# Optimization experiments

Hardware: AMD Instinct MI355X
Metric: run time of the kernel (lower is better)

Reference implementation:

```python
import jax, jax.numpy as jnp
import numpy as np

B, L, D = 32, 2048, 1024
EPS = 1e-5


def setup_inputs() -> dict:
    key = jax.random.key(0)
    k = jax.random.split(key, 4)
    target_mask = jax.random.randint(k[0], (B, L), 0, 2, dtype=jnp.int64)
    x = jax.random.normal(k[1], (B, L, D), dtype=jnp.float32)
    # targets are zeroed out in context (per docstring); makes num_context logic real
    x = x * (1 - target_mask)[:, :, None].astype(jnp.float32)
    W1 = jax.random.normal(k[2], (D, 2 * D), dtype=jnp.float32) * 0.02
    W2 = jax.random.normal(k[3], (2 * D, D), dtype=jnp.float32) * 0.02
    return {
        "context_repr": x,
        "target_mask": target_mask,
        "W1": W1,
        "b1": jnp.zeros((2 * D,), jnp.float32),
        "gamma": jnp.ones((2 * D,), jnp.float32),
        "beta": jnp.zeros((2 * D,), jnp.float32),
        "W2": W2,
        "b2": jnp.zeros((D,), jnp.float32),
    }


def _mlp(x, W1, b1, gamma, beta, W2, b2):
    h = x @ W1 + b1                       # [B, 2D]
    h = jax.nn.gelu(h, approximate=False)  # torch default GELU (erf)
    mu = jnp.mean(h, axis=-1, keepdims=True)
    var = jnp.mean(jnp.square(h - mu), axis=-1, keepdims=True)
    h = (h - mu) * jax.lax.rsqrt(var + EPS) * gamma + beta
    return h @ W2 + b2                    # [B, D]


def reference(context_repr, target_mask, W1, b1, gamma, beta, W2, b2):
    b, l, d = context_repr.shape
    # num_targets is data-dependent but concrete here (eager), matching torch .item()
    ntgt = jnp.sum(target_mask, axis=1)              # [B]
    num_targets = int(jnp.max(ntgt))
    if num_targets == 0:
        return jnp.zeros((b, 1, d), dtype=context_repr.dtype)
    # per-batch masked mean pool: count rows with nonzero L1 norm
    num_ctx = jnp.sum(jnp.sum(jnp.abs(context_repr), axis=-1) > 0, axis=1)  # [B]
    denom = jnp.maximum(num_ctx, 1).astype(context_repr.dtype)[:, None]
    mean = jnp.sum(context_repr, axis=1) / denom
    mean = jnp.where((num_ctx > 0)[:, None], mean, jnp.zeros_like(mean))
    pred = _mlp(mean, W1, b1, gamma, beta, W2, b2)   # [B, D]
    valid = jnp.arange(num_targets)[None, :] < ntgt[:, None]  # [B, T]
    return jnp.where(valid[:, :, None], pred[:, None, :], 0.0)
```

## Files before the change

### kernel.cpp

```cpp
#include <hip/hip_runtime.h>
#include <math.h>

#define BATCH 32
#define LSEQ  2048
#define DIM   1024
#define DIM2  2048

constexpr float EPSF = 1e-5f;

constexpr int CHUNKS = 64;

constexpr int KSEG1 = 32;
constexpr int NSEG1 = DIM / KSEG1;
constexpr int KSEG2 = 32;
constexpr int NSEG2 = DIM2 / KSEG2;

typedef float f4v __attribute__((ext_vector_type(4)));

__global__ __launch_bounds__(256) void k0_compact(const int* __restrict__ m32,
                                                  int* __restrict__ rowlist,
                                                  int* __restrict__ cnt,
                                                  int* __restrict__ ntgt) {
    const int b    = blockIdx.x;
    const int t    = threadIdx.x;
    const int wave = t >> 6, lane = t & 63;

    const int probe = m32[(size_t)b * 2048 + 8 * t + 1];
    __shared__ unsigned long long pbw[4];
    const unsigned long long pb = __ballot(probe != 0);
    if (lane == 0) pbw[wave] = pb;
    __syncthreads();
    const int stride = ((pbw[0] | pbw[1] | pbw[2] | pbw[3]) != 0ull) ? 1 : 2;

    const int base = t * 8;
    int f[8];
    int ls = 0;
    #pragma unroll
    for (int k = 0; k < 8; ++k) {
        f[k] = (m32[((size_t)b * 2048 + base + k) * (size_t)stride] == 0) ? 1 : 0;
        ls += f[k];
    }

    int v = ls;
    #pragma unroll
    for (int o = 1; o < 64; o <<= 1) {
        const int u = __shfl_up(v, o, 64);
        if (lane >= o) v += u;
    }
    __shared__ int wsum[4];
    if (lane == 63) wsum[wave] = v;
    __syncthreads();
    int wbase = 0;
    for (int w = 0; w < wave; ++w) wbase += wsum[w];
    const int excl = wbase + v - ls;

    int c = 0;
    #pragma unroll
    for (int k = 0; k < 8; ++k) {
        if (f[k]) { rowlist[(size_t)b * 2048 + excl + c] = base + k; ++c; }
    }
    if (t == 0) {
        const int tot = wsum[0] + wsum[1] + wsum[2] + wsum[3];
        cnt[b]  = tot;
        ntgt[b] = LSEQ - tot;
    }
}

__global__ __launch_bounds__(256) void k1_gather(const float* __restrict__ x,
                                                 const int* __restrict__ rowlist,
                                                 const int* __restrict__ cnt,
                                                 float* __restrict__ psum) {
    const int chunk = blockIdx.x;
    const int b     = blockIdx.y;
    const int t     = threadIdx.x;

    const int cntb = cnt[b];
    const int nch  = (cntb + 31) >> 5;
    if (chunk >= nch) return;
    const int rbeg = chunk * 32;
    const int rcnt = min(32, cntb - rbeg);

    __shared__ int sidx[32];
    if (t < rcnt) sidx[t] = rowlist[(size_t)b * 2048 + rbeg + t];
    __syncthreads();

    const float* xb = x + (size_t)b * LSEQ * DIM + t * 4;
    float4 acc = make_float4(0.f, 0.f, 0.f, 0.f);

    if (rcnt == 32) {
        #pragma unroll 8
        for (int r = 0; r < 32; ++r) {
            const float4 v = *(const float4*)(xb + (size_t)sidx[r] * DIM);
            acc.x += v.x; acc.y += v.y; acc.z += v.z; acc.w += v.w;
        }
    } else {
        for (int r = 0; r < rcnt; ++r) {
            const float4 v = *(const float4*)(xb + (size_t)sidx[r] * DIM);
            acc.x += v.x; acc.y += v.y; acc.z += v.z; acc.w += v.w;
        }
    }

    *(float4*)(psum + ((size_t)b * CHUNKS + chunk) * DIM + t * 4) = acc;
}

__global__ __launch_bounds__(256) void k2_mean(const float* __restrict__ psum,
                                               const int* __restrict__ cnt,
                                               float* __restrict__ mean) {
    const int b = blockIdx.x;
    const int t = threadIdx.x;
    const int cntb = cnt[b];
    const int nch  = (cntb + 31) >> 5;

    float4 s = make_float4(0.f, 0.f, 0.f, 0.f);
    for (int c = 0; c < nch; ++c) {
        const float4 v = *(const float4*)(psum + ((size_t)b * CHUNKS + c) * DIM + t * 4);
        s.x += v.x; s.y += v.y; s.z += v.z; s.w += v.w;
    }
    const float denom = (float)(cntb > 1 ? cntb : 1);
    float4 m4;
    m4.x = s.x / denom; m4.y = s.y / denom; m4.z = s.z / denom; m4.w = s.w / denom;
    *(float4*)(mean + (size_t)b * DIM + t * 4) = m4;
}

__global__ __launch_bounds__(256) void k3a_h(const float* __restrict__ mean,
                                             const float* __restrict__ W1,
                                             float* __restrict__ p1) {
    const int j  = blockIdx.x * 256 + threadIdx.x;
    const int ks = blockIdx.y;
    const int k0 = ks * KSEG1;

    __shared__ float mlds[BATCH][KSEG1];
    for (int i = threadIdx.x; i < BATCH * KSEG1; i += 256)
        mlds[i >> 5][i & 31] = mean[(size_t)(i >> 5) * DIM + k0 + (i & 31)];
    __syncthreads();

    float acc[BATCH];
    #pragma unroll
    for (int b = 0; b < BATCH; ++b) acc[b] = 0.f;

    #pragma unroll
    for (int k4 = 0; k4 < KSEG1 / 4; ++k4) {
        const float w0 = W1[(size_t)(k0 + 4 * k4 + 0) * DIM2 + j];
        const float w1 = W1[(size_t)(k0 + 4 * k4 + 1) * DIM2 + j];
        const float w2 = W1[(size_t)(k0 + 4 * k4 + 2) * DIM2 + j];
        const float w3 = W1[(size_t)(k0 + 4 * k4 + 3) * DIM2 + j];
        #pragma unroll
        for (int b = 0; b < BATCH; ++b) {
            const float4 m4 = *(const float4*)&mlds[b][k4 * 4];
            acc[b] += m4.x * w0; acc[b] += m4.y * w1;
            acc[b] += m4.z * w2; acc[b] += m4.w * w3;
        }
    }
    #pragma unroll
    for (int b = 0; b < BATCH; ++b)
        p1[((size_t)ks * BATCH + b) * DIM2 + j] = acc[b];
}

__device__ __forceinline__ float wave_sum(float v) {
    #pragma unroll
    for (int o = 32; o > 0; o >>= 1) v += __shfl_down(v, o, 64);
    return v;
}

__global__ __launch_bounds__(256) void k3b_ln(const float* __restrict__ p1,
                                              const float* __restrict__ b1,
                                              const float* __restrict__ gamma,
                                              const float* __restrict__ beta,
                                              float* __restrict__ hn) {
    const int b = blockIdx.x;
    const int t = threadIdx.x;
    const int wave = t >> 6, lane = t & 63;
    __shared__ float red[4];

    float g[8];
    float ls = 0.f;
    #pragma unroll
    for (int i = 0; i < 8; ++i) {
        const int j = t + i * 256;
        float s = b1[j];
        #pragma unroll 8
        for (int ks = 0; ks < NSEG1; ++ks)
            s += p1[((size_t)ks * BATCH + b) * DIM2 + j];
        const float ge = 0.5f * s * (1.f + erff(s * 0.70710678118654752f));
        g[i] = ge;
        ls += ge;
    }

    float w = wave_sum(ls);
    if (lane == 0) red[wave] = w;
    __syncthreads();
    const float mu = (red[0] + red[1] + red[2] + red[3]) * (1.f / (float)DIM2);
    __syncthreads();

    float lv = 0.f;
    #pragma unroll
    for (int i = 0; i < 8; ++i) { const float d = g[i] - mu; lv += d * d; }
    w = wave_sum(lv);
    if (lane == 0) red[wave] = w;
    __syncthreads();
    const float var = (red[0] + red[1] + red[2] + red[3]) * (1.f / (float)DIM2);
    const float rs = rsqrtf(var + EPSF);

    #pragma unroll
    for (int i = 0; i < 8; ++i) {
        const int j = t + i * 256;
        hn[(size_t)b * DIM2 + j] = (g[i] - mu) * rs * gamma[j] + beta[j];
    }
}

__global__ __launch_bounds__(256) void k3c_o(const float* __restrict__ hn,
                                             const float* __restrict__ W2,
                                             float* __restrict__ p2) {
    const int j  = blockIdx.x * 256 + threadIdx.x;
    const int ks = blockIdx.y;
    const int k0 = ks * KSEG2;

    __shared__ float hl[BATCH][KSEG2];
    for (int i = threadIdx.x; i < BATCH * KSEG2; i += 256)
        hl[i >> 5][i & 31] = hn[(size_t)(i >> 5) * DIM2 + k0 + (i & 31)];
    __syncthreads();

    float acc[BATCH];
    #pragma unroll
    for (int b = 0; b < BATCH; ++b) acc[b] = 0.f;

    #pragma unroll
    for (int k4 = 0; k4 < KSEG2 / 4; ++k4) {
        const float w0 = W2[(size_t)(k0 + 4 * k4 + 0) * DIM + j];
        const float w1 = W2[(size_t)(k0 + 4 * k4 + 1) * DIM + j];
        const float w2 = W2[(size_t)(k0 + 4 * k4 + 2) * DIM + j];
        const float w3 = W2[(size_t)(k0 + 4 * k4 + 3) * DIM + j];
        #pragma unroll
        for (int b = 0; b < BATCH; ++b) {
            const float4 h4 = *(const float4*)&hl[b][k4 * 4];
            acc[b] += h4.x * w0; acc[b] += h4.y * w1;
            acc[b] += h4.z * w2; acc[b] += h4.w * w3;
        }
    }
    #pragma unroll
    for (int b = 0; b < BATCH; ++b)
        p2[((size_t)ks * BATCH + b) * DIM + j] = acc[b];
}

__global__ __launch_bounds__(256) void k3d_pred(const float* __restrict__ p2,
                                                const float* __restrict__ b2,
                                                float* __restrict__ pred) {
    const int idx = blockIdx.x * 256 + threadIdx.x;
    const int b = idx >> 10, j = idx & 1023;
    float s = b2[j];
    #pragma unroll 8
    for (int ks = 0; ks < NSEG2; ++ks)
        s += p2[((size_t)ks * BATCH + b) * DIM + j];
    pred[idx] = s;
}

__global__ __launch_bounds__(256) void k4_scatter(const float* __restrict__ pred,
                                                  const int* __restrict__ ntgt,
                                                  f4v* __restrict__ out,
                                                  int T) {
    const int t  = blockIdx.x;
    const int b  = blockIdx.y;
    const int d4 = threadIdx.x;
    f4v v = (f4v)(0.f);
    if (t < ntgt[b]) v = ((const f4v*)pred)[b * 256 + d4];
    __builtin_nontemporal_store(v, &out[((size_t)b * T + t) * 256 + d4]);
}

extern "C" void kernel_launch(void* const* d_in, const int* in_sizes, int n_in,
                              void* d_out, int out_size, void* d_ws, size_t ws_size,
                              hipStream_t stream) {
    const float* x     = (const float*)d_in[0];
    const int*   mask  = (const int*)d_in[1];
    const float* W1    = (const float*)d_in[2];
    const float* b1    = (const float*)d_in[3];
    const float* gamma = (const float*)d_in[4];
    const float* beta  = (const float*)d_in[5];
    const float* W2    = (const float*)d_in[6];
    const float* b2    = (const float*)d_in[7];

    char* ws = (char*)d_ws;
    float* psum = (float*)(ws);
    float* p2   = psum;
    float* p1   = (float*)(ws + (8u  << 20));
    float* mean = (float*)(ws + (16u << 20));
    float* hn   = (float*)(ws + (16u << 20) + (128u << 10));
    float* pred = (float*)(ws + (16u << 20) + (384u << 10));
    int* rowlist= (int*)  (ws + (17u << 20));
    int* cnt    = rowlist + BATCH * LSEQ;
    int* ntgt   = cnt + 64;

    const int T = out_size / (BATCH * DIM);

    k0_compact<<<BATCH, 256, 0, stream>>>(mask, rowlist, cnt, ntgt);
    k1_gather<<<dim3(CHUNKS, BATCH), 256, 0, stream>>>(x, rowlist, cnt, psum);
    k2_mean  <<<BATCH, 256, 0, stream>>>(psum, cnt, mean);
    k3a_h    <<<dim3(DIM2 / 256, NSEG1), 256, 0, stream>>>(mean, W1, p1);
    k3b_ln   <<<BATCH, 256, 0, stream>>>(p1, b1, gamma, beta, hn);
    k3c_o    <<<dim3(DIM / 256, NSEG2), 256, 0, stream>>>(hn, W2, p2);
    k3d_pred <<<(BATCH * DIM) / 256, 256, 0, stream>>>(p2, b2, pred);
    k4_scatter<<<dim3(T, BATCH), 256, 0, stream>>>(pred, ntgt, (f4v*)d_out, T);
}
```

Measured before the change: 113.6 us.

## Fuse mask compaction into gather, mean into first GEMM, pred reduction into scatter

Each gather block now recomputes the per-batch mask scan itself and builds its own 32-row index slice. This removes the separate compaction kernel and its rowlist round-trip. The chunk-sum-to-mean reduction moves into the prologue of the first matmul kernel, and the split-K reduction plus b2 add moves into the scatter kernel. Together these remove three launches and their intermediate buffers. In exchange, the mask scan runs redundantly in every gather block, and the scatter grid shrinks to 8 blocks per batch, each writing many rows in a loop, which may lower store parallelism on the large output write.

```diff
diff --git a/kernel.cpp b/kernel.cpp
--- a/kernel.cpp
+++ b/kernel.cpp
@@ -15,18 +15,25 @@
 constexpr int KSEG2 = 32;
 constexpr int NSEG2 = DIM2 / KSEG2;
 
+constexpr int K4_BLKS = 8;
+
 typedef float f4v __attribute__((ext_vector_type(4)));
 
-__global__ __launch_bounds__(256) void k0_compact(const int* __restrict__ m32,
-                                                  int* __restrict__ rowlist,
-                                                  int* __restrict__ cnt,
-                                                  int* __restrict__ ntgt) {
-    const int b    = blockIdx.x;
-    const int t    = threadIdx.x;
-    const int wave = t >> 6, lane = t & 63;
+__global__ __launch_bounds__(256) void k1_fused(const float* __restrict__ x,
+                                                const int* __restrict__ m32,
+                                                float* __restrict__ psum,
+                                                int* __restrict__ cnt,
+                                                int* __restrict__ ntgt) {
+    const int chunk = blockIdx.x;
+    const int b     = blockIdx.y;
+    const int t     = threadIdx.x;
+    const int wave  = t >> 6, lane = t & 63;
+
+    __shared__ unsigned long long pbw[4];
+    __shared__ int wsum[4];
+    __shared__ int sidx[32];
 
     const int probe = m32[(size_t)b * 2048 + 8 * t + 1];
-    __shared__ unsigned long long pbw[4];
     const unsigned long long pb = __ballot(probe != 0);
     if (lane == 0) pbw[wave] = pb;
     __syncthreads();
@@ -40,89 +47,56 @@
         f[k] = (m32[((size_t)b * 2048 + base + k) * (size_t)stride] == 0) ? 1 : 0;
         ls += f[k];
     }
-
     int v = ls;
     #pragma unroll
     for (int o = 1; o < 64; o <<= 1) {
         const int u = __shfl_up(v, o, 64);
         if (lane >= o) v += u;
     }
-    __shared__ int wsum[4];
     if (lane == 63) wsum[wave] = v;
     __syncthreads();
     int wbase = 0;
     for (int w = 0; w < wave; ++w) wbase += wsum[w];
-    const int excl = wbase + v - ls;
-
-    int c = 0;
-    #pragma unroll
-    for (int k = 0; k < 8; ++k) {
-        if (f[k]) { rowlist[(size_t)b * 2048 + excl + c] = base + k; ++c; }
-    }
-    if (t == 0) {
-        const int tot = wsum[0] + wsum[1] + wsum[2] + wsum[3];
-        cnt[b]  = tot;
-        ntgt[b] = LSEQ - tot;
-    }
-}
-
-__global__ __launch_bounds__(256) void k1_gather(const float* __restrict__ x,
-                                                 const int* __restrict__ rowlist,
-                                                 const int* __restrict__ cnt,
-                                                 float* __restrict__ psum) {
-    const int chunk = blockIdx.x;
-    const int b     = blockIdx.y;
-    const int t     = threadIdx.x;
-
-    const int cntb = cnt[b];
-    const int nch  = (cntb + 31) >> 5;
+    const int excl  = wbase + v - ls;
+    const int total = wsum[0] + wsum[1] + wsum[2] + wsum[3];
+
+    if (chunk == 0 && t == 0) { cnt[b] = total; ntgt[b] = LSEQ - total; }
+
+    const int nch = (total + 31) >> 5;
     if (chunk >= nch) return;
     const int rbeg = chunk * 32;
-    const int rcnt = min(32, cntb - rbeg);
-
-    __shared__ int sidx[32];
-    if (t < rcnt) sidx[t] = rowlist[(size_t)b * 2048 + rbeg + t];
+    const int rcnt = min(32, total - rbeg);
+
+    int c = 0;
+    #pragma unroll
+    for (int k = 0; k < 8; ++k) {
+        if (f[k]) {
+            const int pos = excl + c;
+            if (pos >= rbeg && pos < rbeg + 32) sidx[pos - rbeg] = base + k;
+            ++c;
+        }
+    }
     __syncthreads();
 
     const float* xb = x + (size_t)b * LSEQ * DIM + t * 4;
     float4 acc = make_float4(0.f, 0.f, 0.f, 0.f);
-
     if (rcnt == 32) {
         #pragma unroll 8
         for (int r = 0; r < 32; ++r) {
-            const float4 v = *(const float4*)(xb + (size_t)sidx[r] * DIM);
-            acc.x += v.x; acc.y += v.y; acc.z += v.z; acc.w += v.w;
+            const float4 vv = *(const float4*)(xb + (size_t)sidx[r] * DIM);
+            acc.x += vv.x; acc.y += vv.y; acc.z += vv.z; acc.w += vv.w;
         }
     } else {
         for (int r = 0; r < rcnt; ++r) {
-            const float4 v = *(const float4*)(xb + (size_t)sidx[r] * DIM);
-            acc.x += v.x; acc.y += v.y; acc.z += v.z; acc.w += v.w;
-        }
-    }
-
+            const float4 vv = *(const float4*)(xb + (size_t)sidx[r] * DIM);
+            acc.x += vv.x; acc.y += vv.y; acc.z += vv.z; acc.w += vv.w;
+        }
+    }
     *(float4*)(psum + ((size_t)b * CHUNKS + chunk) * DIM + t * 4) = acc;
 }
 
-__global__ __launch_bounds__(256) void k2_mean(const float* __restrict__ psum,
-                                               const int* __restrict__ cnt,
-                                               float* __restrict__ mean) {
-    const int b = blockIdx.x;
-    const int t = threadIdx.x;
-    const int cntb = cnt[b];
-    const int nch  = (cntb + 31) >> 5;
-
-    float4 s = make_float4(0.f, 0.f, 0.f, 0.f);
-    for (int c = 0; c < nch; ++c) {
-        const float4 v = *(const float4*)(psum + ((size_t)b * CHUNKS + c) * DIM + t * 4);
-        s.x += v.x; s.y += v.y; s.z += v.z; s.w += v.w;
-    }
-    const float denom = (float)(cntb > 1 ? cntb : 1);
-    float4 m4;
-    m4.x = s.x / denom; m4.y = s.y / denom; m4.z = s.z / denom; m4.w = s.w / denom;
-    *(float4*)(mean + (size_t)b * DIM + t * 4) = m4;
-}
-
-__global__ __launch_bounds__(256) void k3a_h(const float* __restrict__ mean,
+__global__ __launch_bounds__(256) void k3a_h(const float* __restrict__ psum,
+                                             const int* __restrict__ cnt,
                                              const float* __restrict__ W1,
                                              float* __restrict__ p1) {
     const int j  = blockIdx.x * 256 + threadIdx.x;
@@ -130,8 +104,19 @@
     const int k0 = ks * KSEG1;
 
     __shared__ float mlds[BATCH][KSEG1];
-    for (int i = threadIdx.x; i < BATCH * KSEG1; i += 256)
-        mlds[i >> 5][i & 31] = mean[(size_t)(i >> 5) * DIM + k0 + (i & 31)];
+    {
+        const int b  = threadIdx.x >> 3;
+        const int kq = threadIdx.x & 7;
+        const int cb = cnt[b];
+        const int nch = (cb + 31) >> 5;
+        float4 s = make_float4(0.f, 0.f, 0.f, 0.f);
+        for (int c = 0; c < nch; ++c) {
+            const float4 vv = *(const float4*)(psum + ((size_t)b * CHUNKS + c) * DIM + k0 + kq * 4);
+            s.x += vv.x; s.y += vv.y; s.z += vv.z; s.w += vv.w;
+        }
+        const float inv = 1.f / (float)(cb > 1 ? cb : 1);
+        *(float4*)&mlds[b][kq * 4] = make_float4(s.x * inv, s.y * inv, s.z * inv, s.w * inv);
+    }
     __syncthreads();
 
     float acc[BATCH];
@@ -242,28 +227,33 @@
         p2[((size_t)ks * BATCH + b) * DIM + j] = acc[b];
 }
 
-__global__ __launch_bounds__(256) void k3d_pred(const float* __restrict__ p2,
-                                                const float* __restrict__ b2,
-                                                float* __restrict__ pred) {
-    const int idx = blockIdx.x * 256 + threadIdx.x;
-    const int b = idx >> 10, j = idx & 1023;
-    float s = b2[j];
-    #pragma unroll 8
-    for (int ks = 0; ks < NSEG2; ++ks)
-        s += p2[((size_t)ks * BATCH + b) * DIM + j];
-    pred[idx] = s;
-}
-
-__global__ __launch_bounds__(256) void k4_scatter(const float* __restrict__ pred,
+__global__ __launch_bounds__(256) void k4_scatter(const float* __restrict__ p2,
+                                                  const float* __restrict__ b2,
                                                   const int* __restrict__ ntgt,
                                                   f4v* __restrict__ out,
                                                   int T) {
-    const int t  = blockIdx.x;
+    const int g  = blockIdx.x;
     const int b  = blockIdx.y;
     const int d4 = threadIdx.x;
-    f4v v = (f4v)(0.f);
-    if (t < ntgt[b]) v = ((const f4v*)pred)[b * 256 + d4];
-    __builtin_nontemporal_store(v, &out[((size_t)b * T + t) * 256 + d4]);
+    const int n  = ntgt[b];
+
+    float4 s = *(const float4*)(b2 + d4 * 4);
+    #pragma unroll 8
+    for (int ks = 0; ks < NSEG2; ++ks) {
+        const float4 vv = *(const float4*)(p2 + ((size_t)ks * BATCH + b) * DIM + d4 * 4);
+        s.x += vv.x; s.y += vv.y; s.z += vv.z; s.w += vv.w;
+    }
+    f4v p; p.x = s.x; p.y = s.y; p.z = s.z; p.w = s.w;
+    const f4v z = (f4v)(0.f);
+
+    const int R  = (T + K4_BLKS - 1) / K4_BLKS;
+    const int t0 = g * R;
+    f4v* o = out + ((size_t)b * T + t0) * 256 + d4;
+    for (int r = 0; r < R; ++r) {
+        const int tt = t0 + r;
+        if (tt >= T) break;
+        __builtin_nontemporal_store((tt < n) ? p : z, &o[(size_t)r * 256]);
+    }
 }
 
 extern "C" void kernel_launch(void* const* d_in, const int* in_sizes, int n_in,
@@ -282,21 +272,15 @@
     float* psum = (float*)(ws);
     float* p2   = psum;
     float* p1   = (float*)(ws + (8u  << 20));
-    float* mean = (float*)(ws + (16u << 20));
-    float* hn   = (float*)(ws + (16u << 20) + (128u << 10));
-    float* pred = (float*)(ws + (16u << 20) + (384u << 10));
-    int* rowlist= (int*)  (ws + (17u << 20));
-    int* cnt    = rowlist + BATCH * LSEQ;
-    int* ntgt   = cnt + 64;
+    float* hn   = (float*)(ws + (16u << 20));
+    int*   cnt  = (int*)  (ws + (16u << 20) + (512u << 10));
+    int*   ntgt = cnt + 64;
 
     const int T = out_size / (BATCH * DIM);
 
-    k0_compact<<<BATCH, 256, 0, stream>>>(mask, rowlist, cnt, ntgt);
-    k1_gather<<<dim3(CHUNKS, BATCH), 256, 0, stream>>>(x, rowlist, cnt, psum);
-    k2_mean  <<<BATCH, 256, 0, stream>>>(psum, cnt, mean);
-    k3a_h    <<<dim3(DIM2 / 256, NSEG1), 256, 0, stream>>>(mean, W1, p1);
+    k1_fused <<<dim3(CHUNKS, BATCH), 256, 0, stream>>>(x, mask, psum, cnt, ntgt);
+    k3a_h    <<<dim3(DIM2 / 256, NSEG1), 256, 0, stream>>>(psum, cnt, W1, p1);
     k3b_ln   <<<BATCH, 256, 0, stream>>>(p1, b1, gamma, beta, hn);
     k3c_o    <<<dim3(DIM / 256, NSEG2), 256, 0, stream>>>(hn, W2, p2);
-    k3d_pred <<<(BATCH * DIM) / 256, 256, 0, stream>>>(p2, b2, pred);
-    k4_scatter<<<dim3(T, BATCH), 256, 0, stream>>>(pred, ntgt, (f4v*)d_out, T);
-}
+    k4_scatter<<<dim3(K4_BLKS, BATCH), 256, 0, stream>>>(p2, b2, ntgt, (f4v*)d_out, T);
+}
```

After: 124.7 us. 9.8% more time.
